# Kernel optimization log

Hardware: AMD Instinct MI355X
Metric: run time of the kernel (lower is better)

Reference implementation:

```python
import jax, jax.numpy as jnp
import numpy as np

B, S, D, H = 2, 2048, 1024, 16
HD = D // H  # head_dim = 64


def setup_inputs() -> dict:
    key = jax.random.key(0)
    ks = jax.random.split(key, 6)
    scale = 0.02
    return {
        "x": jax.random.normal(ks[0], (B, S, D), dtype=jnp.float32),
        "wq": jax.random.normal(ks[1], (D, D), dtype=jnp.float32) * scale,  # torch Linear weight [out,in]
        "wk": jax.random.normal(ks[2], (D, D), dtype=jnp.float32) * scale,
        "wv": jax.random.normal(ks[3], (D, D), dtype=jnp.float32) * scale,
        "wo": jax.random.normal(ks[4], (D, D), dtype=jnp.float32) * scale,
        "bo": jnp.zeros((D,), dtype=jnp.float32),
    }


def reference(x, wq, wk, wv, wo, bo):
    b, t, d = x.shape
    # projections (torch nn.Linear: x @ W.T), split into heads -> [b, h, t, hd]
    def split_heads(y):
        return y.reshape(b, t, H, HD).transpose(0, 2, 1, 3)

    q = split_heads(x @ wq.T)
    k = split_heads(x @ wk.T)
    v = split_heads(x @ wv.T)

    scores = jnp.einsum("bhqd,bhkd->bhqk", q, k)  # [b,h,t,t]
    causal = jnp.triu(jnp.ones((t, t), dtype=bool), k=1)
    scores = jnp.where(causal, -jnp.inf, scores)
    attn = jax.nn.softmax(scores / jnp.sqrt(jnp.asarray(HD, scores.dtype)), axis=-1)
    # dropout p=0.0 -> identity (eval-mode reference)
    ctx = jnp.einsum("bhqk,bhkd->bhqd", attn, v)
    ctx = ctx.transpose(0, 2, 1, 3).reshape(b, t, d)
    return ctx @ wo.T + bo
```

## Files before the change

kernel.cpp:

```cpp
#include <hip/hip_runtime.h>
#include <hip/hip_bf16.h>
#include <stdint.h>
#include <math.h>

#define NH   16
#define HDIM 64
#define SEQ  2048
#define DM   1024
#define NB   2
#define MTOK (NB * SEQ)

typedef __bf16 bf16x8 __attribute__((ext_vector_type(8)));
typedef float  f32x4  __attribute__((ext_vector_type(4)));

__device__ __forceinline__ unsigned short f2bf(float f) {
  union { float f; unsigned int u; } c; c.f = f;
  unsigned int u = c.u;
  return (unsigned short)((u + 0x7FFFu + ((u >> 16) & 1u)) >> 16);
}
__device__ __forceinline__ float bf2f(unsigned short s) {
  union { unsigned int u; float f; } c; c.u = ((unsigned int)s) << 16;
  return c.f;
}
__device__ __forceinline__ unsigned int pk2bf(float a, float b) {
  __hip_bfloat162 h = __float22bfloat162_rn(float2{a, b});
  return *reinterpret_cast<unsigned int*>(&h);
}

__device__ __forceinline__ void async_copy16(const void* g, void* l) {
  __builtin_amdgcn_global_load_lds((__attribute__((address_space(1))) void*)g,
                                   (__attribute__((address_space(3))) void*)l,
                                   16, 0, 0);
}

__global__ void cast_all(const float* __restrict__ x,  const float* __restrict__ wq,
                         const float* __restrict__ wk, const float* __restrict__ wv,
                         const float* __restrict__ wo,
                         unsigned short* __restrict__ xb,
                         unsigned short* __restrict__ wqkvb,
                         unsigned short* __restrict__ wob) {
  const int seg = blockIdx.y;
  const float* src;
  unsigned short* dst;
  int n4;
  if (seg == 0)      { src = x;  dst = xb;                  n4 = MTOK * DM / 4; }
  else if (seg == 1) { src = wq; dst = wqkvb;               n4 = DM * DM / 4; }
  else if (seg == 2) { src = wk; dst = wqkvb + DM * DM;     n4 = DM * DM / 4; }
  else if (seg == 3) { src = wv; dst = wqkvb + 2 * DM * DM; n4 = DM * DM / 4; }
  else               { src = wo; dst = wob;                 n4 = DM * DM / 4; }
  const int i = blockIdx.x * blockDim.x + threadIdx.x;
  if (i >= n4) return;
  float4 v = reinterpret_cast<const float4*>(src)[i];
  uint2 o;
  o.x = pk2bf(v.x, v.y); o.y = pk2bf(v.z, v.w);
  reinterpret_cast<uint2*>(dst)[i] = o;
}

#define QSCALE 0.1803368801111244f
template <int MODE>
__global__ __launch_bounds__(256, 2) void gemm_bt(
    const unsigned short* __restrict__ A,
    const unsigned short* __restrict__ B,
    unsigned short* __restrict__ qo, unsigned short* __restrict__ ko,
    unsigned short* __restrict__ vo,
    float* __restrict__ co, const float* __restrict__ bias,
    int M, int N, int K) {
  __shared__ __align__(16) unsigned short As[128 * 32];
  __shared__ __align__(16) unsigned short Bs[128 * 32];

  const int tid  = threadIdx.x;
  const int lane = tid & 63;
  const int wave = tid >> 6;
  const int l15  = lane & 15;
  const int quad = lane >> 4;
  const int wm   = (wave >> 1) * 64;
  const int wn   = (wave & 1) * 64;
  const int m0   = blockIdx.x * 128;
  const int n0   = blockIdx.y * 128;

  f32x4 acc[4][4];
#pragma unroll
  for (int a = 0; a < 4; ++a)
#pragma unroll
    for (int b = 0; b < 4; ++b) acc[a][b] = f32x4{0.f, 0.f, 0.f, 0.f};

  for (int k0 = 0; k0 < K; k0 += 32) {
    __syncthreads();
#pragma unroll
    for (int s = 0; s < 2; ++s) {
      const int c   = tid + s * 256;
      const int row = c >> 2;
      const int col = (c & 3) * 8;
      unsigned short* lA = As + ((size_t)wave * 64 + s * 256) * 8;
      unsigned short* lB = Bs + ((size_t)wave * 64 + s * 256) * 8;
      async_copy16(A + (size_t)(m0 + row) * K + k0 + col, lA);
      async_copy16(B + (size_t)(n0 + row) * K + k0 + col, lB);
    }
    __syncthreads();

    bf16x8 af[4], bfr[4];
#pragma unroll
    for (int t = 0; t < 4; ++t) {
      af[t]  = *reinterpret_cast<const bf16x8*>(As + (wm + t * 16 + l15) * 32 + quad * 8);
      bfr[t] = *reinterpret_cast<const bf16x8*>(Bs + (wn + t * 16 + l15) * 32 + quad * 8);
    }
#pragma unroll
    for (int ti = 0; ti < 4; ++ti)
#pragma unroll
      for (int tj = 0; tj < 4; ++tj)
        acc[ti][tj] = __builtin_amdgcn_mfma_f32_16x16x32_bf16(af[ti], bfr[tj], acc[ti][tj], 0, 0, 0);
  }

#pragma unroll
  for (int ti = 0; ti < 4; ++ti) {
#pragma unroll
    for (int tj = 0; tj < 4; ++tj) {
      const int mb = m0 + wm + ti * 16 + quad * 4;
      const int n  = n0 + wn + tj * 16 + l15;
      if (MODE == 0) {
        const int which = n >> 10;
        const int n1 = n & 1023;
        const int h = n1 >> 6, d = n1 & 63;
        const int b = mb >> 11, s = mb & 2047;
        if (which == 0) {
          const size_t idx = ((size_t)(b * NH + h) * SEQ + s) * HDIM + d;
#pragma unroll
          for (int r = 0; r < 4; ++r) qo[idx + (size_t)r * HDIM] = f2bf(acc[ti][tj][r] * QSCALE);
        } else if (which == 1) {
          const size_t idx = ((size_t)(b * NH + h) * SEQ + s) * HDIM + d;
#pragma unroll
          for (int r = 0; r < 4; ++r) ko[idx + (size_t)r * HDIM] = f2bf(acc[ti][tj][r]);
        } else {
          const size_t idx = ((size_t)(b * NH + h) * HDIM + d) * SEQ + s;
          uint2 pk;
          pk.x = pk2bf(acc[ti][tj][0], acc[ti][tj][1]);
          pk.y = pk2bf(acc[ti][tj][2], acc[ti][tj][3]);
          *reinterpret_cast<uint2*>(vo + idx) = pk;
        }
      } else {
#pragma unroll
        for (int r = 0; r < 4; ++r)
          co[(size_t)(mb + r) * N + n] = acc[ti][tj][r] + bias[n];
      }
    }
  }
}

#define KST 72
#define PST 72

__global__ __launch_bounds__(256, 5) void flash_attn_mfma(
    const unsigned short* __restrict__ Qb,
    const unsigned short* __restrict__ Kb,
    const unsigned short* __restrict__ Vtg,
    unsigned short* __restrict__ ctx,
    unsigned short* __restrict__ pO,
    float* __restrict__ pL) {
  __shared__ __align__(16) unsigned short Ks[64 * KST];
  __shared__ __align__(16) unsigned short Vt[64 * KST];
  __shared__ __align__(16) unsigned short Pt[4][16 * PST];

  const int tid  = threadIdx.x;
  const int bh   = blockIdx.y;
  const int lane = tid & 63;
  const int wave = tid >> 6;
  const int l15  = lane & 15;
  const int quad = lane >> 4;

  int qt, chunk, nch;
  {
    const int x = blockIdx.x;
    if (x < 12)      { qt = x;                 chunk = 0;            nch = 1; }
    else if (x < 36) { qt = 12 + (x - 12) / 2; chunk = (x - 12) % 2; nch = 2; }
    else             { qt = 24 + (x - 36) / 3; chunk = (x - 36) % 3; nch = 3; }
  }
  const int q0 = qt * 64;
  const int c0 = chunk * 12;
  const int c1 = min(qt, c0 + 11);

  const size_t baseQK = (size_t)bh * SEQ * HDIM;
  const size_t baseV  = (size_t)bh * HDIM * SEQ;

  const int srow = tid >> 3;
  const int scol = (tid & 7) * 8;

  bf16x8 qf[2];
  {
    const unsigned short* qp = Qb + baseQK + (size_t)(q0 + wave * 16 + l15) * HDIM + quad * 8;
    qf[0] = *reinterpret_cast<const bf16x8*>(qp);
    qf[1] = *reinterpret_cast<const bf16x8*>(qp + 32);
  }

  float l_acc = 0.f;
  f32x4 o[4];
#pragma unroll
  for (int td = 0; td < 4; ++td) o[td] = f32x4{0.f, 0.f, 0.f, 0.f};

  for (int kt = c0; kt <= c1; ++kt) {
    __syncthreads();
    {
      const uint4 k0v = *reinterpret_cast<const uint4*>(Kb + baseQK + (size_t)(kt * 64 + srow) * HDIM + scol);
      const uint4 k1v = *reinterpret_cast<const uint4*>(Kb + baseQK + (size_t)(kt * 64 + srow + 32) * HDIM + scol);
      const uint4 v0v = *reinterpret_cast<const uint4*>(Vtg + baseV + (size_t)srow * SEQ + kt * 64 + scol);
      const uint4 v1v = *reinterpret_cast<const uint4*>(Vtg + baseV + (size_t)(srow + 32) * SEQ + kt * 64 + scol);
      *reinterpret_cast<uint4*>(&Ks[srow * KST + scol]) = k0v;
      *reinterpret_cast<uint4*>(&Ks[(srow + 32) * KST + scol]) = k1v;
      *reinterpret_cast<uint4*>(&Vt[srow * KST + scol]) = v0v;
      *reinterpret_cast<uint4*>(&Vt[(srow + 32) * KST + scol]) = v1v;
    }
    __syncthreads();

    const int tmax = (kt == qt) ? wave : 3;

    f32x4 st[4];
#pragma unroll
    for (int t = 0; t < 4; ++t) st[t] = f32x4{-INFINITY, -INFINITY, -INFINITY, -INFINITY};
#pragma unroll
    for (int t = 0; t < 4; ++t) {
      if (t <= tmax) {
        f32x4 c = f32x4{0.f, 0.f, 0.f, 0.f};
        const int krow = (t * 16 + l15) * KST;
        const bf16x8 kf0 = *reinterpret_cast<const bf16x8*>(&Ks[krow + quad * 8]);
        const bf16x8 kf1 = *reinterpret_cast<const bf16x8*>(&Ks[krow + 32 + quad * 8]);
        c = __builtin_amdgcn_mfma_f32_16x16x32_bf16(kf0, qf[0], c, 0, 0, 0);
        c = __builtin_amdgcn_mfma_f32_16x16x32_bf16(kf1, qf[1], c, 0, 0, 0);
        if (kt == qt && t == wave) {
#pragma unroll
          for (int r = 0; r < 4; ++r)
            if (quad * 4 + r > l15) c[r] = -INFINITY;
        }
        st[t] = c;
      }
    }

#pragma unroll
    for (int t = 0; t < 4; ++t) {
      const float p0 = exp2f(st[t][0]);
      const float p1 = exp2f(st[t][1]);
      const float p2 = exp2f(st[t][2]);
      const float p3 = exp2f(st[t][3]);
      l_acc += (p0 + p1) + (p2 + p3);
      uint2 pk;
      pk.x = pk2bf(p0, p1);
      pk.y = pk2bf(p2, p3);
      *reinterpret_cast<uint2*>(&Pt[wave][l15 * PST + t * 16 + quad * 4]) = pk;
    }

    const int smax = (kt == qt && wave < 2) ? 0 : 1;
#pragma unroll
    for (int sv = 0; sv < 2; ++sv) {
      if (sv <= smax) {
        const bf16x8 pf = *reinterpret_cast<const bf16x8*>(&Pt[wave][l15 * PST + sv * 32 + quad * 8]);
#pragma unroll
        for (int td = 0; td < 4; ++td) {
          const bf16x8 vf = *reinterpret_cast<const bf16x8*>(&Vt[(td * 16 + l15) * KST + sv * 32 + quad * 8]);
          o[td] = __builtin_amdgcn_mfma_f32_16x16x32_bf16(pf, vf, o[td], 0, 0, 0);
        }
      }
    }
  }

  float l_s = l_acc;
  l_s += __shfl_xor(l_s, 16, 64);
  l_s += __shfl_xor(l_s, 32, 64);

  if (nch == 1) {
    const float linv = 1.f / l_s;
    const int b = bh >> 4, h = bh & 15;
#pragma unroll
    for (int r = 0; r < 4; ++r) {
      const float lr = __shfl(linv, quad * 4 + r, 64);
      const int sr = q0 + wave * 16 + quad * 4 + r;
      const size_t ob = (size_t)(b * SEQ + sr) * DM + h * HDIM + l15;
#pragma unroll
      for (int td = 0; td < 4; ++td)
        ctx[ob + td * 16] = f2bf(o[td][r] * lr);
    }
  } else {
    const int pb = (qt < 24) ? 2 * (qt - 12) : 24 + 3 * (qt - 24);
    const int pidx = bh * 48 + pb + chunk;
    if (quad == 0) pL[pidx * 64 + wave * 16 + l15] = l_s;
    unsigned short* po = pO + (size_t)pidx * 4096;
#pragma unroll
    for (int r = 0; r < 4; ++r) {
      const int ql = wave * 16 + quad * 4 + r;
#pragma unroll
      for (int td = 0; td < 4; ++td)
        po[ql * 64 + td * 16 + l15] = f2bf(o[td][r]);
    }
  }
}

__global__ __launch_bounds__(256, 8) void attn_reduce(
    const unsigned short* __restrict__ pO, const float* __restrict__ pL,
    unsigned short* __restrict__ ctx) {
  const int x = blockIdx.x;
  int qt, pb, nch;
  if (x < 12) { qt = 12 + x; pb = 2 * x;            nch = 2; }
  else        { qt = 24 + (x - 12); pb = 24 + 3 * (x - 12); nch = 3; }
  const int bh = blockIdx.y;
  const int b = bh >> 4, h = bh & 15;
  const int pidx = bh * 48 + pb;

  const int tid = threadIdx.x;
  const int ql  = tid >> 2;
  const int d0  = (tid & 3) * 16;

  float acc[16];
#pragma unroll
  for (int e = 0; e < 16; ++e) acc[e] = 0.f;
  float lsum = 0.f;

  for (int c = 0; c < nch; ++c) {
    lsum += pL[(pidx + c) * 64 + ql];
    const unsigned short* src = pO + (size_t)(pidx + c) * 4096 + ql * 64 + d0;
    const uint4 v0 = *reinterpret_cast<const uint4*>(src);
    const uint4 v1 = *reinterpret_cast<const uint4*>(src + 8);
    const unsigned short* u = reinterpret_cast<const unsigned short*>(&v0);
    const unsigned short* w = reinterpret_cast<const unsigned short*>(&v1);
#pragma unroll
    for (int e = 0; e < 8; ++e) { acc[e] += bf2f(u[e]); acc[8 + e] += bf2f(w[e]); }
  }

  const float linv = 1.f / lsum;
  unsigned int outw[8];
#pragma unroll
  for (int e = 0; e < 8; ++e)
    outw[e] = pk2bf(acc[2 * e] * linv, acc[2 * e + 1] * linv);
  unsigned short* dst = ctx + (size_t)(b * SEQ + qt * 64 + ql) * DM + h * HDIM + d0;
  *reinterpret_cast<uint4*>(dst)     = *reinterpret_cast<uint4*>(&outw[0]);
  *reinterpret_cast<uint4*>(dst + 8) = *reinterpret_cast<uint4*>(&outw[4]);
}

extern "C" void kernel_launch(void* const* d_in, const int* in_sizes, int n_in,
                              void* d_out, int out_size, void* d_ws, size_t ws_size,
                              hipStream_t stream) {
  const float* x  = (const float*)d_in[0];
  const float* wq = (const float*)d_in[1];
  const float* wk = (const float*)d_in[2];
  const float* wv = (const float*)d_in[3];
  const float* wo = (const float*)d_in[4];
  const float* bo = (const float*)d_in[5];
  float* out = (float*)d_out;

  char* ws = (char*)d_ws;
  unsigned short* xb    = (unsigned short*)(ws);
  unsigned short* wqkvb = (unsigned short*)(ws + (8ull  << 20));
  unsigned short* wob   = (unsigned short*)(ws + (14ull << 20));
  unsigned short* Qb    = (unsigned short*)(ws + (16ull << 20));
  unsigned short* Kb    = (unsigned short*)(ws + (24ull << 20));
  unsigned short* Vtg   = (unsigned short*)(ws + (32ull << 20));
  unsigned short* ctxb  = (unsigned short*)(ws + (40ull << 20));
  unsigned short* pO    = (unsigned short*)(ws);
  float*          pL    = (float*)(ws + (12ull << 20));

  dim3 gc(4096, 5);
  cast_all<<<gc, 256, 0, stream>>>(x, wq, wk, wv, wo, xb, wqkvb, wob);

  dim3 g1(MTOK / 128, (3 * DM) / 128);
  gemm_bt<0><<<g1, 256, 0, stream>>>(xb, wqkvb, Qb, Kb, Vtg, nullptr, nullptr,
                                     MTOK, 3 * DM, DM);

  dim3 g2(60, NB * NH);
  flash_attn_mfma<<<g2, 256, 0, stream>>>(Qb, Kb, Vtg, ctxb, pO, pL);

  dim3 gr(20, NB * NH);
  attn_reduce<<<gr, 256, 0, stream>>>(pO, pL, ctxb);

  dim3 g3(MTOK / 128, DM / 128);
  gemm_bt<1><<<g3, 256, 0, stream>>>(ctxb, wob, nullptr, nullptr, nullptr, out, bo,
                                     MTOK, DM, DM);
}
```

Measured before the change: 201.3 us.

## Keep attention P in registers via 16x16x16 MFMA, shrink out-proj tile, flatten cast

The flash attention kernel now feeds the exponentiated score fragment straight from registers into a 16x16x16 bf16 MFMA against V. This removes the per-wave LDS staging buffer for P and its write/read round trip, and occupancy is raised to 6 blocks. The output projection GEMM uses a 64-wide N tile so it launches twice as many blocks. The cast kernel is flattened into a 1D grid with no idle blocks. The risks are more, smaller MFMAs in the attention loop and a lower compute-to-load ratio in the output GEMM.

```diff
diff --git a/kernel.cpp b/kernel.cpp
--- a/kernel.cpp
+++ b/kernel.cpp
@@ -11,6 +11,8 @@
 #define MTOK (NB * SEQ)
 
 typedef __bf16 bf16x8 __attribute__((ext_vector_type(8)));
+typedef __bf16 bf16x4 __attribute__((ext_vector_type(4)));
+typedef short  short4v __attribute__((ext_vector_type(4)));
 typedef float  f32x4  __attribute__((ext_vector_type(4)));
 
 __device__ __forceinline__ unsigned short f2bf(float f) {
@@ -25,6 +27,15 @@
 __device__ __forceinline__ unsigned int pk2bf(float a, float b) {
   __hip_bfloat162 h = __float22bfloat162_rn(float2{a, b});
   return *reinterpret_cast<unsigned int*>(&h);
+}
+
+__device__ __forceinline__ f32x4 mfma16(short4v a, short4v b, f32x4 c) {
+#if __has_builtin(__builtin_amdgcn_mfma_f32_16x16x16_bf16)
+  return __builtin_amdgcn_mfma_f32_16x16x16_bf16(
+      __builtin_bit_cast(bf16x4, a), __builtin_bit_cast(bf16x4, b), c, 0, 0, 0);
+#else
+  return __builtin_amdgcn_mfma_f32_16x16x16bf16_1k(a, b, c, 0, 0, 0);
+#endif
 }
 
 __device__ __forceinline__ void async_copy16(const void* g, void* l) {
@@ -39,21 +50,25 @@
                          unsigned short* __restrict__ xb,
                          unsigned short* __restrict__ wqkvb,
                          unsigned short* __restrict__ wob) {
-  const int seg = blockIdx.y;
-  const float* src;
-  unsigned short* dst;
-  int n4;
-  if (seg == 0)      { src = x;  dst = xb;                  n4 = MTOK * DM / 4; }
-  else if (seg == 1) { src = wq; dst = wqkvb;               n4 = DM * DM / 4; }
-  else if (seg == 2) { src = wk; dst = wqkvb + DM * DM;     n4 = DM * DM / 4; }
-  else if (seg == 3) { src = wv; dst = wqkvb + 2 * DM * DM; n4 = DM * DM / 4; }
-  else               { src = wo; dst = wob;                 n4 = DM * DM / 4; }
-  const int i = blockIdx.x * blockDim.x + threadIdx.x;
-  if (i >= n4) return;
-  float4 v = reinterpret_cast<const float4*>(src)[i];
+  const int i = blockIdx.x * 256 + threadIdx.x;
+  float4 v;
+  uint2* dstp;
+  int idx;
+  if (i < (1 << 20)) {
+    v = reinterpret_cast<const float4*>(x)[i];
+    dstp = reinterpret_cast<uint2*>(xb); idx = i;
+  } else {
+    const int j = i - (1 << 20);
+    const int seg = j >> 18;
+    idx = j & ((1 << 18) - 1);
+    const float* w = (seg == 0) ? wq : (seg == 1) ? wk : (seg == 2) ? wv : wo;
+    v = reinterpret_cast<const float4*>(w)[idx];
+    if (seg < 3) { dstp = reinterpret_cast<uint2*>(wqkvb); idx += seg * (1 << 18); }
+    else         { dstp = reinterpret_cast<uint2*>(wob); }
+  }
   uint2 o;
   o.x = pk2bf(v.x, v.y); o.y = pk2bf(v.z, v.w);
-  reinterpret_cast<uint2*>(dst)[i] = o;
+  dstp[idx] = o;
 }
 
 #define QSCALE 0.1803368801111244f
@@ -65,8 +80,11 @@
     unsigned short* __restrict__ vo,
     float* __restrict__ co, const float* __restrict__ bias,
     int M, int N, int K) {
+  constexpr int BN = (MODE == 0) ? 128 : 64;
+  constexpr int TJ = BN / 32;
+  constexpr int RB = BN * 4 / 256;
   __shared__ __align__(16) unsigned short As[128 * 32];
-  __shared__ __align__(16) unsigned short Bs[128 * 32];
+  __shared__ __align__(16) unsigned short Bs[BN * 32];
 
   const int tid  = threadIdx.x;
   const int lane = tid & 63;
@@ -74,15 +92,15 @@
   const int l15  = lane & 15;
   const int quad = lane >> 4;
   const int wm   = (wave >> 1) * 64;
-  const int wn   = (wave & 1) * 64;
+  const int wn   = (wave & 1) * (BN / 2);
   const int m0   = blockIdx.x * 128;
-  const int n0   = blockIdx.y * 128;
-
-  f32x4 acc[4][4];
+  const int n0   = blockIdx.y * BN;
+
+  f32x4 acc[4][TJ];
 #pragma unroll
   for (int a = 0; a < 4; ++a)
 #pragma unroll
-    for (int b = 0; b < 4; ++b) acc[a][b] = f32x4{0.f, 0.f, 0.f, 0.f};
+    for (int b = 0; b < TJ; ++b) acc[a][b] = f32x4{0.f, 0.f, 0.f, 0.f};
 
   for (int k0 = 0; k0 < K; k0 += 32) {
     __syncthreads();
@@ -92,29 +110,36 @@
       const int row = c >> 2;
       const int col = (c & 3) * 8;
       unsigned short* lA = As + ((size_t)wave * 64 + s * 256) * 8;
+      async_copy16(A + (size_t)(m0 + row) * K + k0 + col, lA);
+    }
+#pragma unroll
+    for (int s = 0; s < RB; ++s) {
+      const int c   = tid + s * 256;
+      const int row = c >> 2;
+      const int col = (c & 3) * 8;
       unsigned short* lB = Bs + ((size_t)wave * 64 + s * 256) * 8;
-      async_copy16(A + (size_t)(m0 + row) * K + k0 + col, lA);
       async_copy16(B + (size_t)(n0 + row) * K + k0 + col, lB);
     }
     __syncthreads();
 
-    bf16x8 af[4], bfr[4];
-#pragma unroll
-    for (int t = 0; t < 4; ++t) {
+    bf16x8 af[4], bfr[TJ];
+#pragma unroll
+    for (int t = 0; t < 4; ++t)
       af[t]  = *reinterpret_cast<const bf16x8*>(As + (wm + t * 16 + l15) * 32 + quad * 8);
+#pragma unroll
+    for (int t = 0; t < TJ; ++t)
       bfr[t] = *reinterpret_cast<const bf16x8*>(Bs + (wn + t * 16 + l15) * 32 + quad * 8);
-    }
 #pragma unroll
     for (int ti = 0; ti < 4; ++ti)
 #pragma unroll
-      for (int tj = 0; tj < 4; ++tj)
+      for (int tj = 0; tj < TJ; ++tj)
         acc[ti][tj] = __builtin_amdgcn_mfma_f32_16x16x32_bf16(af[ti], bfr[tj], acc[ti][tj], 0, 0, 0);
   }
 
 #pragma unroll
   for (int ti = 0; ti < 4; ++ti) {
 #pragma unroll
-    for (int tj = 0; tj < 4; ++tj) {
+    for (int tj = 0; tj < TJ; ++tj) {
       const int mb = m0 + wm + ti * 16 + quad * 4;
       const int n  = n0 + wn + tj * 16 + l15;
       if (MODE == 0) {
@@ -147,9 +172,8 @@
 }
 
 #define KST 72
-#define PST 72
-
-__global__ __launch_bounds__(256, 5) void flash_attn_mfma(
+
+__global__ __launch_bounds__(256, 6) void flash_attn_mfma(
     const unsigned short* __restrict__ Qb,
     const unsigned short* __restrict__ Kb,
     const unsigned short* __restrict__ Vtg,
@@ -158,7 +182,6 @@
     float* __restrict__ pL) {
   __shared__ __align__(16) unsigned short Ks[64 * KST];
   __shared__ __align__(16) unsigned short Vt[64 * KST];
-  __shared__ __align__(16) unsigned short Pt[4][16 * PST];
 
   const int tid  = threadIdx.x;
   const int bh   = blockIdx.y;
@@ -212,9 +235,6 @@
 
     const int tmax = (kt == qt) ? wave : 3;
 
-    f32x4 st[4];
-#pragma unroll
-    for (int t = 0; t < 4; ++t) st[t] = f32x4{-INFINITY, -INFINITY, -INFINITY, -INFINITY};
 #pragma unroll
     for (int t = 0; t < 4; ++t) {
       if (t <= tmax) {
@@ -229,32 +249,21 @@
           for (int r = 0; r < 4; ++r)
             if (quad * 4 + r > l15) c[r] = -INFINITY;
         }
-        st[t] = c;
-      }
-    }
-
-#pragma unroll
-    for (int t = 0; t < 4; ++t) {
-      const float p0 = exp2f(st[t][0]);
-      const float p1 = exp2f(st[t][1]);
-      const float p2 = exp2f(st[t][2]);
-      const float p3 = exp2f(st[t][3]);
-      l_acc += (p0 + p1) + (p2 + p3);
-      uint2 pk;
-      pk.x = pk2bf(p0, p1);
-      pk.y = pk2bf(p2, p3);
-      *reinterpret_cast<uint2*>(&Pt[wave][l15 * PST + t * 16 + quad * 4]) = pk;
-    }
-
-    const int smax = (kt == qt && wave < 2) ? 0 : 1;
-#pragma unroll
-    for (int sv = 0; sv < 2; ++sv) {
-      if (sv <= smax) {
-        const bf16x8 pf = *reinterpret_cast<const bf16x8*>(&Pt[wave][l15 * PST + sv * 32 + quad * 8]);
+
+        const float p0 = exp2f(c[0]);
+        const float p1 = exp2f(c[1]);
+        const float p2 = exp2f(c[2]);
+        const float p3 = exp2f(c[3]);
+        l_acc += (p0 + p1) + (p2 + p3);
+        union { uint2 u; short4v s; } pf;
+        pf.u.x = pk2bf(p0, p1);
+        pf.u.y = pk2bf(p2, p3);
+
 #pragma unroll
         for (int td = 0; td < 4; ++td) {
-          const bf16x8 vf = *reinterpret_cast<const bf16x8*>(&Vt[(td * 16 + l15) * KST + sv * 32 + quad * 8]);
-          o[td] = __builtin_amdgcn_mfma_f32_16x16x32_bf16(pf, vf, o[td], 0, 0, 0);
+          const short4v vf = *reinterpret_cast<const short4v*>(
+              &Vt[(td * 16 + l15) * KST + t * 16 + quad * 4]);
+          o[td] = mfma16(pf.s, vf, o[td]);
         }
       }
     }
@@ -354,8 +363,7 @@
   unsigned short* pO    = (unsigned short*)(ws);
   float*          pL    = (float*)(ws + (12ull << 20));
 
-  dim3 gc(4096, 5);
-  cast_all<<<gc, 256, 0, stream>>>(x, wq, wk, wv, wo, xb, wqkvb, wob);
+  cast_all<<<8192, 256, 0, stream>>>(x, wq, wk, wv, wo, xb, wqkvb, wob);
 
   dim3 g1(MTOK / 128, (3 * DM) / 128);
   gemm_bt<0><<<g1, 256, 0, stream>>>(xb, wqkvb, Qb, Kb, Vtg, nullptr, nullptr,
@@ -367,7 +375,7 @@
   dim3 gr(20, NB * NH);
   attn_reduce<<<gr, 256, 0, stream>>>(pO, pL, ctxb);
 
-  dim3 g3(MTOK / 128, DM / 128);
+  dim3 g3(MTOK / 128, DM / 64);
   gemm_bt<1><<<g3, 256, 0, stream>>>(ctxb, wob, nullptr, nullptr, nullptr, out, bo,
                                      MTOK, DM, DM);
 }
```

Measured after the change: 187.7 us. 6.7% less time.
